# Optimization experiments

Measured on AMD Instinct MI355X. Metric: run time of the kernel, lower is better.

## Reference

```python
import jax, jax.numpy as jnp
import numpy as np

D_MODEL = 512
NUM_HEADS = 8
HEAD_DIM = D_MODEL // NUM_HEADS
NEG_INF = -1e9


def setup_inputs() -> dict:
    key = jax.random.key(0)
    ks = jax.random.split(key, 12)
    B, S = 4, 2048
    std = 1.0 / np.sqrt(D_MODEL)
    inp = {
        "query": jax.random.normal(ks[0], (B, S, D_MODEL), jnp.float32),
        "key": jax.random.normal(ks[1], (B, S, D_MODEL), jnp.float32),
        "value": jax.random.normal(ks[2], (B, S, D_MODEL), jnp.float32),
        "mask": jax.random.randint(ks[3], (B, 1, S, S), 0, 2, jnp.int32),
        "Wq": jax.random.normal(ks[4], (D_MODEL, D_MODEL), jnp.float32) * std,
        "bq": jnp.zeros((D_MODEL,), jnp.float32),
        "Wk": jax.random.normal(ks[5], (D_MODEL, D_MODEL), jnp.float32) * std,
        "bk": jnp.zeros((D_MODEL,), jnp.float32),
        "Wv": jax.random.normal(ks[6], (D_MODEL, D_MODEL), jnp.float32) * std,
        "bv": jnp.zeros((D_MODEL,), jnp.float32),
        "Wo": jax.random.normal(ks[7], (D_MODEL, D_MODEL), jnp.float32) * std,
        "bo": jnp.zeros((D_MODEL,), jnp.float32),
    }
    return inp


def _split_heads(x):
    B, S, _ = x.shape
    return x.reshape(B, S, NUM_HEADS, HEAD_DIM).transpose(0, 2, 1, 3)  # [B,H,S,Dh]


def reference(query, key, value, mask, Wq, bq, Wk, bk, Wv, bv, Wo, bo):
    B, S, _ = query.shape
    q = _split_heads(query @ Wq + bq)
    k = _split_heads(key @ Wk + bk)
    v = _split_heads(value @ Wv + bv)
    # scores: [B,H,S,S]
    scores = jnp.einsum("bhqd,bhkd->bhqk", q, k) / jnp.sqrt(jnp.float32(HEAD_DIM))
    scores = jnp.where(mask == 0, jnp.float32(NEG_INF), scores)
    attn = jax.nn.softmax(scores, axis=-1)  # dropout p=0 -> identity
    out = jnp.einsum("bhqk,bhkd->bhqd", attn, v)
    out = out.transpose(0, 2, 1, 3).reshape(B, S, D_MODEL)
    return out @ Wo + bo
```

## Files before the change

kernel.cpp:

```cpp
#include <hip/hip_runtime.h>

typedef unsigned short u16;
typedef __attribute__((ext_vector_type(4))) float f32x4;
typedef __attribute__((ext_vector_type(8))) short s16x8;
typedef __attribute__((ext_vector_type(4))) unsigned short u16x4;

__device__ __forceinline__ u16 f2bf(float f) {
    union { float f; unsigned u; } v; v.f = f;
    unsigned r = v.u + 0x7fffu + ((v.u >> 16) & 1u);
    return (u16)(r >> 16);
}
__device__ __forceinline__ float bf2f(u16 h) {
    union { unsigned u; float f; } v; v.u = ((unsigned)h) << 16;
    return v.f;
}
__device__ __forceinline__ void gload16(const void* g, void* lds_uniform) {
    __builtin_amdgcn_global_load_lds(
        (const __attribute__((address_space(1))) void*)g,
        (__attribute__((address_space(3))) void*)lds_uniform, 16, 0, 0);
}
__device__ __forceinline__ f32x4 mfma16(s16x8 a, s16x8 b, f32x4 c) {
    return __builtin_amdgcn_mfma_f32_16x16x32_bf16(a, b, c, 0, 0, 0);
}

__global__ void cvtbf3(const float4* __restrict__ q, const float4* __restrict__ k,
                       const float4* __restrict__ v, u16x4* __restrict__ out) {
    int i = blockIdx.x * 256 + threadIdx.x;
    int sel = i >> 20;
    int j = i & 0xFFFFF;
    const float4* in = (sel == 0) ? q : (sel == 1) ? k : v;
    float4 f = in[j];
    u16x4 o;
    o[0] = f2bf(f.x); o[1] = f2bf(f.y); o[2] = f2bf(f.z); o[3] = f2bf(f.w);
    out[i] = o;
}

__global__ void wtrans(const float* __restrict__ W0, const float* __restrict__ W1,
                       const float* __restrict__ W2, const float* __restrict__ W3,
                       u16* __restrict__ T0, u16* __restrict__ T1,
                       u16* __restrict__ T2, u16* __restrict__ T3) {
    const float* W; u16* T;
    switch (blockIdx.z) {
        case 0: W = W0; T = T0; break;
        case 1: W = W1; T = T1; break;
        case 2: W = W2; T = T2; break;
        default: W = W3; T = T3; break;
    }
    __shared__ float tile[32][33];
    const int tx = threadIdx.x & 31, ty = threadIdx.x >> 5;
    const int k0 = blockIdx.y * 32, n0 = blockIdx.x * 32;
#pragma unroll
    for (int r = 0; r < 32; r += 8) tile[ty + r][tx] = W[(k0 + ty + r) * 512 + n0 + tx];
    __syncthreads();
#pragma unroll
    for (int r = 0; r < 32; r += 8) T[(n0 + ty + r) * 512 + k0 + tx] = f2bf(tile[tx][ty + r]);
}

__global__ void packmask(const int* __restrict__ mask, unsigned* __restrict__ bits) {
    int i = blockIdx.x * 256 + threadIdx.x;
    int v = mask[i];
    unsigned long long bal = __ballot(v != 0);
    if ((threadIdx.x & 63) == 0) {
        uint2 w; w.x = (unsigned)bal; w.y = (unsigned)(bal >> 32);
        *(uint2*)&bits[i >> 5] = w;
    }
}

template <int BIAS_ROW, int OUT_F32>
__global__ __launch_bounds__(256, 2) void gemm_bt(
    const u16* __restrict__ A, const u16* __restrict__ Bt0, const u16* __restrict__ Bt1,
    const float* __restrict__ bias0, const float* __restrict__ bias1,
    void* __restrict__ Cout, int M, int N, int K, int ysplit) {
    const u16* Bt = (blockIdx.y < (unsigned)ysplit) ? Bt0 : Bt1;
    const float* bias = (blockIdx.y < (unsigned)ysplit) ? bias0 : bias1;
    __shared__ u16 As[128 * 32];
    __shared__ u16 Bs[128 * 32];
    const int t = threadIdx.x, l = t & 63, w = t >> 6;
    const int lr = l & 15, lg = l >> 4;
    const int m0 = blockIdx.y * 128, n0 = blockIdx.x * 128;
    const int wr = w >> 1, wc = w & 1;
    f32x4 acc[4][4] = {};

    const int c0 = t, c1 = 256 + t;
    const int ar0 = c0 >> 2, ac0 = (c0 & 3) * 8;
    const int ar1 = c1 >> 2, ac1 = (c1 & 3) * 8;

    for (int kk = 0; kk < K; kk += 32) {
        __syncthreads();
        gload16(A + (m0 + ar0) * K + kk + ac0, As + (w * 64) * 8);
        gload16(A + (m0 + ar1) * K + kk + ac1, As + (256 + w * 64) * 8);
        gload16(Bt + (n0 + ar0) * K + kk + ac0, Bs + (w * 64) * 8);
        gload16(Bt + (n0 + ar1) * K + kk + ac1, Bs + (256 + w * 64) * 8);
        __syncthreads();
        s16x8 af[4], bf[4];
#pragma unroll
        for (int m = 0; m < 4; ++m)
            af[m] = *(const s16x8*)&As[(wr * 64 + m * 16 + lr) * 32 + lg * 8];
#pragma unroll
        for (int n = 0; n < 4; ++n)
            bf[n] = *(const s16x8*)&Bs[(wc * 64 + n * 16 + lr) * 32 + lg * 8];
#pragma unroll
        for (int m = 0; m < 4; ++m)
#pragma unroll
            for (int n = 0; n < 4; ++n) acc[m][n] = mfma16(af[m], bf[n], acc[m][n]);
    }

#pragma unroll
    for (int n = 0; n < 4; ++n) {
        const int cg = n0 + wc * 64 + n * 16 + lr;
        const float bcol = BIAS_ROW ? 0.f : bias[cg];
#pragma unroll
        for (int m = 0; m < 4; ++m) {
            const int rbase = m0 + wr * 64 + m * 16 + lg * 4;
#pragma unroll
            for (int j = 0; j < 4; ++j) {
                const int rg = rbase + j;
                float v = acc[m][n][j] + (BIAS_ROW ? bias[rg] : bcol);
                if (OUT_F32) ((float*)Cout)[rg * N + cg] = v;
                else         ((u16*)Cout)[rg * N + cg] = f2bf(v);
            }
        }
    }
}

__global__ __launch_bounds__(256, 4) void attn_fwd(
    const u16* __restrict__ Qp, const u16* __restrict__ Kp,
    const u16* __restrict__ Vt, const unsigned* __restrict__ mbits,
    u16* __restrict__ AO) {
    constexpr int S = 2048;
    const int qt = blockIdx.x, bh = blockIdx.y;
    const int b = bh >> 3, h = bh & 7;
    const int t = threadIdx.x, l = t & 63, w = t >> 6;
    const int lr = l & 15, lg = l >> 4;

    __shared__ u16 Ks[64 * 64];
    __shared__ u16 Vs[64 * 64];
    __shared__ u16 Ps[4][16 * 64];

    const int q0 = qt * 64 + w * 16;
    const int bS = b * S;

    s16x8 qf[2];
#pragma unroll
    for (int ks = 0; ks < 2; ++ks) {
        s16x8 v = *(const s16x8*)&Qp[(bS + q0 + lr) * 512 + h * 64 + ks * 32 + lg * 8];
#pragma unroll
        for (int j = 0; j < 8; ++j) v[j] = (short)f2bf(bf2f((u16)v[j]) * 0.125f);
        qf[ks] = v;
    }

    f32x4 po[4] = {};
    float lrun[4] = {0.f, 0.f, 0.f, 0.f};

    const int kc0 = t, kc1 = 256 + t;
    const int krow0 = kc0 >> 3, kcol0 = ((kc0 & 7) ^ (krow0 & 7)) * 8;
    const int krow1 = kc1 >> 3, kcol1 = ((kc1 & 7) ^ (krow1 & 7)) * 8;

    for (int kt0 = 0; kt0 < S; kt0 += 64) {
        __syncthreads();
        gload16(&Kp[(bS + kt0 + krow0) * 512 + h * 64 + kcol0], &Ks[w * 512]);
        gload16(&Kp[(bS + kt0 + krow1) * 512 + h * 64 + kcol1], &Ks[2048 + w * 512]);
        gload16(&Vt[(h * 64 + krow0) * (4 * S) + bS + kt0 + kcol0], &Vs[w * 512]);
        gload16(&Vt[(h * 64 + krow1) * (4 * S) + bS + kt0 + kcol1], &Vs[2048 + w * 512]);

        uint2 mw[4];
#pragma unroll
        for (int jj = 0; jj < 4; ++jj)
            mw[jj] = *(const uint2*)&mbits[(bS + q0 + lg * 4 + jj) * 64 + (kt0 >> 5)];
        __syncthreads();

        f32x4 sc[4];
#pragma unroll
        for (int nk = 0; nk < 4; ++nk) sc[nk] = f32x4{0.f, 0.f, 0.f, 0.f};
#pragma unroll
        for (int nk = 0; nk < 4; ++nk) {
            const int ktc = nk * 16 + lr;
            const int sw = (ktc & 7) << 4;
            s16x8 k0 = *(const s16x8*)((const char*)Ks + ((ktc * 128 + lg * 16) ^ sw));
            s16x8 k1 = *(const s16x8*)((const char*)Ks + ((ktc * 128 + 64 + lg * 16) ^ sw));
            sc[nk] = mfma16(qf[0], k0, sc[nk]);
            sc[nk] = mfma16(qf[1], k1, sc[nk]);
        }

#pragma unroll
        for (int nk = 0; nk < 4; ++nk) {
            const unsigned bp = ((nk & 1) << 4) + lr;
#pragma unroll
            for (int jj = 0; jj < 4; ++jj) {
                const unsigned word = (nk >> 1) ? mw[jj].y : mw[jj].x;
                const float s = ((word >> bp) & 1u) ? sc[nk][jj] : -1e9f;
                sc[nk][jj] = __expf(s);
            }
        }
#pragma unroll
        for (int jj = 0; jj < 4; ++jj)
            lrun[jj] += (sc[0][jj] + sc[1][jj]) + (sc[2][jj] + sc[3][jj]);

#pragma unroll
        for (int nk = 0; nk < 4; ++nk) {
            const int ktc = nk * 16 + lr;
#pragma unroll
            for (int jj = 0; jj < 4; ++jj) {
                const int qloc = lg * 4 + jj;
                const int byte = (qloc * 128 + ktc * 2) ^ ((qloc & 7) << 4);
                *(u16*)((char*)&Ps[w][0] + byte) = f2bf(sc[nk][jj]);
            }
        }

        s16x8 pa[2];
#pragma unroll
        for (int k2 = 0; k2 < 2; ++k2) {
            const int byte = (lr * 128 + k2 * 64 + lg * 16) ^ ((lr & 7) << 4);
            pa[k2] = *(const s16x8*)((const char*)&Ps[w][0] + byte);
        }
#pragma unroll
        for (int dn = 0; dn < 4; ++dn) {
            const int d = dn * 16 + lr;
            const int sw = (d & 7) << 4;
            s16x8 v0 = *(const s16x8*)((const char*)Vs + ((d * 128 + lg * 16) ^ sw));
            s16x8 v1 = *(const s16x8*)((const char*)Vs + ((d * 128 + 64 + lg * 16) ^ sw));
            po[dn] = mfma16(pa[0], v0, po[dn]);
            po[dn] = mfma16(pa[1], v1, po[dn]);
        }
    }

#pragma unroll
    for (int jj = 0; jj < 4; ++jj) {
        float s = lrun[jj];
        s += __shfl_xor(s, 1);
        s += __shfl_xor(s, 2);
        s += __shfl_xor(s, 4);
        s += __shfl_xor(s, 8);
        const float inv = 1.f / s;
        const int q = q0 + lg * 4 + jj;
#pragma unroll
        for (int dn = 0; dn < 4; ++dn)
            AO[(bS + q) * 512 + h * 64 + dn * 16 + lr] = f2bf(po[dn][jj] * inv);
    }
}

extern "C" void kernel_launch(void* const* d_in, const int* in_sizes, int n_in,
                              void* d_out, int out_size, void* d_ws, size_t ws_size,
                              hipStream_t stream) {
    (void)in_sizes; (void)n_in; (void)out_size; (void)ws_size;
    const float* query = (const float*)d_in[0];
    const float* key   = (const float*)d_in[1];
    const float* value = (const float*)d_in[2];
    const int*   mask  = (const int*)d_in[3];
    const float* Wq = (const float*)d_in[4];
    const float* bq = (const float*)d_in[5];
    const float* Wk = (const float*)d_in[6];
    const float* bk = (const float*)d_in[7];
    const float* Wv = (const float*)d_in[8];
    const float* bv = (const float*)d_in[9];
    const float* Wo = (const float*)d_in[10];
    const float* bo = (const float*)d_in[11];

    char* ws = (char*)d_ws;
    const size_t MB = 1ull << 20;
    u16* qb  = (u16*)(ws);
    u16* vb  = (u16*)(ws + 16 * MB);
    u16* WqT = (u16*)(ws + 24 * MB);
    u16* WkT = (u16*)(ws + 24 * MB + 512 * 1024);
    u16* WvT = (u16*)(ws + 25 * MB);
    u16* WoT = (u16*)(ws + 25 * MB + 512 * 1024);
    unsigned* mb = (unsigned*)(ws + 26 * MB);
    u16* Qp = (u16*)(ws + 28 * MB);
    u16* Vt = (u16*)(ws + 44 * MB);
    u16* AO = (u16*)(ws + 52 * MB);

    cvtbf3<<<12288, 256, 0, stream>>>((const float4*)query, (const float4*)key,
                                      (const float4*)value, (u16x4*)qb);
    wtrans<<<dim3(16, 16, 4), 256, 0, stream>>>(Wq, Wk, Wv, Wo, WqT, WkT, WvT, WoT);
    packmask<<<65536, 256, 0, stream>>>(mask, mb);

    gemm_bt<0, 0><<<dim3(4, 128), 256, 0, stream>>>(qb, WqT, WkT, bq, bk, Qp,
                                                    16384, 512, 512, 64);
    gemm_bt<1, 0><<<dim3(64, 4), 256, 0, stream>>>(WvT, vb, vb, bv, bv, Vt,
                                                   512, 8192, 512, 999);

    attn_fwd<<<dim3(32, 32), 256, 0, stream>>>(Qp, Qp + 8192 * 512, Vt, mb, AO);

    gemm_bt<0, 1><<<dim3(4, 64), 256, 0, stream>>>(AO, WoT, WoT, bo, bo,
                                                   (float*)d_out, 8192, 512, 512, 999);
}
```

Baseline: 159.5 us.

## Fuse preprocessing kernels, shrink GEMM tiles, and use exp2 with folded log2e scale

```diff
diff --git a/kernel.cpp b/kernel.cpp
--- a/kernel.cpp
+++ b/kernel.cpp
@@ -14,6 +14,13 @@
     union { unsigned u; float f; } v; v.u = ((unsigned)h) << 16;
     return v.f;
 }
+__device__ __forceinline__ float fexp2(float x) {
+#if __has_builtin(__builtin_amdgcn_exp2f)
+    return __builtin_amdgcn_exp2f(x);
+#else
+    return exp2f(x);
+#endif
+}
 __device__ __forceinline__ void gload16(const void* g, void* lds_uniform) {
     __builtin_amdgcn_global_load_lds(
         (const __attribute__((address_space(1))) void*)g,
@@ -23,101 +30,101 @@
     return __builtin_amdgcn_mfma_f32_16x16x32_bf16(a, b, c, 0, 0, 0);
 }
 
-__global__ void cvtbf3(const float4* __restrict__ q, const float4* __restrict__ k,
-                       const float4* __restrict__ v, u16x4* __restrict__ out) {
-    int i = blockIdx.x * 256 + threadIdx.x;
-    int sel = i >> 20;
-    int j = i & 0xFFFFF;
-    const float4* in = (sel == 0) ? q : (sel == 1) ? k : v;
-    float4 f = in[j];
-    u16x4 o;
-    o[0] = f2bf(f.x); o[1] = f2bf(f.y); o[2] = f2bf(f.z); o[3] = f2bf(f.w);
-    out[i] = o;
-}
-
-__global__ void wtrans(const float* __restrict__ W0, const float* __restrict__ W1,
-                       const float* __restrict__ W2, const float* __restrict__ W3,
-                       u16* __restrict__ T0, u16* __restrict__ T1,
-                       u16* __restrict__ T2, u16* __restrict__ T3) {
-    const float* W; u16* T;
-    switch (blockIdx.z) {
-        case 0: W = W0; T = T0; break;
-        case 1: W = W1; T = T1; break;
-        case 2: W = W2; T = T2; break;
-        default: W = W3; T = T3; break;
-    }
+__global__ void prep(const float4* __restrict__ q, const float4* __restrict__ k,
+                     const float4* __restrict__ v, u16x4* __restrict__ qkv,
+                     const float* __restrict__ Wq, const float* __restrict__ Wk,
+                     const float* __restrict__ Wv, const float* __restrict__ Wo,
+                     u16* __restrict__ WqT, u16* __restrict__ WkT,
+                     u16* __restrict__ WvT, u16* __restrict__ WoT,
+                     const int* __restrict__ mask, unsigned* __restrict__ bits) {
     __shared__ float tile[32][33];
-    const int tx = threadIdx.x & 31, ty = threadIdx.x >> 5;
-    const int k0 = blockIdx.y * 32, n0 = blockIdx.x * 32;
-#pragma unroll
-    for (int r = 0; r < 32; r += 8) tile[ty + r][tx] = W[(k0 + ty + r) * 512 + n0 + tx];
-    __syncthreads();
-#pragma unroll
-    for (int r = 0; r < 32; r += 8) T[(n0 + ty + r) * 512 + k0 + tx] = f2bf(tile[tx][ty + r]);
-}
-
-__global__ void packmask(const int* __restrict__ mask, unsigned* __restrict__ bits) {
-    int i = blockIdx.x * 256 + threadIdx.x;
-    int v = mask[i];
-    unsigned long long bal = __ballot(v != 0);
-    if ((threadIdx.x & 63) == 0) {
-        uint2 w; w.x = (unsigned)bal; w.y = (unsigned)(bal >> 32);
-        *(uint2*)&bits[i >> 5] = w;
-    }
-}
-
-template <int BIAS_ROW, int OUT_F32>
-__global__ __launch_bounds__(256, 2) void gemm_bt(
+    const int bid = blockIdx.x, tid = threadIdx.x;
+    if (bid < 12288) {
+        int i = bid * 256 + tid;
+        int sel = i >> 20, j = i & 0xFFFFF;
+        const float4* in = (sel == 0) ? q : (sel == 1) ? k : v;
+        float4 f = in[j];
+        u16x4 o;
+        o[0] = f2bf(f.x); o[1] = f2bf(f.y); o[2] = f2bf(f.z); o[3] = f2bf(f.w);
+        qkv[i] = o;
+    } else if (bid < 13312) {
+        int idx = bid - 12288;
+        int bz = idx >> 8, rem = idx & 255, by = rem >> 4, bx = rem & 15;
+        const float* W; u16* T;
+        switch (bz) {
+            case 0: W = Wq; T = WqT; break;
+            case 1: W = Wk; T = WkT; break;
+            case 2: W = Wv; T = WvT; break;
+            default: W = Wo; T = WoT; break;
+        }
+        const int tx = tid & 31, ty = tid >> 5;
+        const int k0 = by * 32, n0 = bx * 32;
+#pragma unroll
+        for (int r = 0; r < 32; r += 8) tile[ty + r][tx] = W[(k0 + ty + r) * 512 + n0 + tx];
+        __syncthreads();
+#pragma unroll
+        for (int r = 0; r < 32; r += 8) T[(n0 + ty + r) * 512 + k0 + tx] = f2bf(tile[tx][ty + r]);
+    } else {
+        int i = (bid - 13312) * 256 + tid;
+        int m = mask[i];
+        unsigned long long bal = __ballot(m != 0);
+        if ((tid & 63) == 0) {
+            uint2 w2; w2.x = (unsigned)bal; w2.y = (unsigned)(bal >> 32);
+            *(uint2*)&bits[i >> 5] = w2;
+        }
+    }
+}
+
+template <int BM, int BIAS_ROW, int OUT_F32>
+__global__ __launch_bounds__(256, 4) void gemm_bt(
     const u16* __restrict__ A, const u16* __restrict__ Bt0, const u16* __restrict__ Bt1,
     const float* __restrict__ bias0, const float* __restrict__ bias1,
     void* __restrict__ Cout, int M, int N, int K, int ysplit) {
+    constexpr int MR = BM / 32;
     const u16* Bt = (blockIdx.y < (unsigned)ysplit) ? Bt0 : Bt1;
     const float* bias = (blockIdx.y < (unsigned)ysplit) ? bias0 : bias1;
-    __shared__ u16 As[128 * 32];
-    __shared__ u16 Bs[128 * 32];
+    __shared__ u16 As[BM * 32];
+    __shared__ u16 Bs[64 * 32];
     const int t = threadIdx.x, l = t & 63, w = t >> 6;
     const int lr = l & 15, lg = l >> 4;
-    const int m0 = blockIdx.y * 128, n0 = blockIdx.x * 128;
+    const int m0 = blockIdx.y * BM, n0 = blockIdx.x * 64;
     const int wr = w >> 1, wc = w & 1;
-    f32x4 acc[4][4] = {};
-
-    const int c0 = t, c1 = 256 + t;
-    const int ar0 = c0 >> 2, ac0 = (c0 & 3) * 8;
-    const int ar1 = c1 >> 2, ac1 = (c1 & 3) * 8;
+    f32x4 acc[MR][2] = {};
+    const int ar = t >> 2, ac = (t & 3) * 8;
 
     for (int kk = 0; kk < K; kk += 32) {
         __syncthreads();
-        gload16(A + (m0 + ar0) * K + kk + ac0, As + (w * 64) * 8);
-        gload16(A + (m0 + ar1) * K + kk + ac1, As + (256 + w * 64) * 8);
-        gload16(Bt + (n0 + ar0) * K + kk + ac0, Bs + (w * 64) * 8);
-        gload16(Bt + (n0 + ar1) * K + kk + ac1, Bs + (256 + w * 64) * 8);
-        __syncthreads();
-        s16x8 af[4], bf[4];
-#pragma unroll
-        for (int m = 0; m < 4; ++m)
-            af[m] = *(const s16x8*)&As[(wr * 64 + m * 16 + lr) * 32 + lg * 8];
-#pragma unroll
-        for (int n = 0; n < 4; ++n)
-            bf[n] = *(const s16x8*)&Bs[(wc * 64 + n * 16 + lr) * 32 + lg * 8];
-#pragma unroll
-        for (int m = 0; m < 4; ++m)
-#pragma unroll
-            for (int n = 0; n < 4; ++n) acc[m][n] = mfma16(af[m], bf[n], acc[m][n]);
-    }
-
-#pragma unroll
-    for (int n = 0; n < 4; ++n) {
-        const int cg = n0 + wc * 64 + n * 16 + lr;
+        gload16(A + (m0 + ar) * K + kk + ac, As + w * 512);
+        if (BM == 128)
+            gload16(A + (m0 + 64 + ar) * K + kk + ac, As + 2048 + w * 512);
+        gload16(Bt + (n0 + ar) * K + kk + ac, Bs + w * 512);
+        __syncthreads();
+        s16x8 af[MR], bfr[2];
+#pragma unroll
+        for (int m = 0; m < MR; ++m)
+            af[m] = *(const s16x8*)&As[(wr * (BM / 2) + m * 16 + lr) * 32 + lg * 8];
+#pragma unroll
+        for (int n = 0; n < 2; ++n)
+            bfr[n] = *(const s16x8*)&Bs[(wc * 32 + n * 16 + lr) * 32 + lg * 8];
+#pragma unroll
+        for (int m = 0; m < MR; ++m)
+#pragma unroll
+            for (int n = 0; n < 2; ++n) acc[m][n] = mfma16(af[m], bfr[n], acc[m][n]);
+    }
+
+#pragma unroll
+    for (int n = 0; n < 2; ++n) {
+        const int cg = n0 + wc * 32 + n * 16 + lr;
         const float bcol = BIAS_ROW ? 0.f : bias[cg];
 #pragma unroll
-        for (int m = 0; m < 4; ++m) {
-            const int rbase = m0 + wr * 64 + m * 16 + lg * 4;
+        for (int m = 0; m < MR; ++m) {
+            const int rbase = m0 + wr * (BM / 2) + m * 16 + lg * 4;
 #pragma unroll
             for (int j = 0; j < 4; ++j) {
                 const int rg = rbase + j;
-                float v = acc[m][n][j] + (BIAS_ROW ? bias[rg] : bcol);
-                if (OUT_F32) ((float*)Cout)[rg * N + cg] = v;
-                else         ((u16*)Cout)[rg * N + cg] = f2bf(v);
+                float val = acc[m][n][j] + (BIAS_ROW ? bias[rg] : bcol);
+                if (OUT_F32) ((float*)Cout)[(size_t)rg * N + cg] = val;
+                else         ((u16*)Cout)[(size_t)rg * N + cg] = f2bf(val);
             }
         }
     }
@@ -145,7 +152,7 @@
     for (int ks = 0; ks < 2; ++ks) {
         s16x8 v = *(const s16x8*)&Qp[(bS + q0 + lr) * 512 + h * 64 + ks * 32 + lg * 8];
 #pragma unroll
-        for (int j = 0; j < 8; ++j) v[j] = (short)f2bf(bf2f((u16)v[j]) * 0.125f);
+        for (int j = 0; j < 8; ++j) v[j] = (short)f2bf(bf2f((u16)v[j]) * 0.1803368851f);
         qf[ks] = v;
     }
 
@@ -189,7 +196,7 @@
             for (int jj = 0; jj < 4; ++jj) {
                 const unsigned word = (nk >> 1) ? mw[jj].y : mw[jj].x;
                 const float s = ((word >> bp) & 1u) ? sc[nk][jj] : -1e9f;
-                sc[nk][jj] = __expf(s);
+                sc[nk][jj] = fexp2(s);
             }
         }
 #pragma unroll
@@ -213,6 +220,7 @@
             const int byte = (lr * 128 + k2 * 64 + lg * 16) ^ ((lr & 7) << 4);
             pa[k2] = *(const s16x8*)((const char*)&Ps[w][0] + byte);
         }
+
 #pragma unroll
         for (int dn = 0; dn < 4; ++dn) {
             const int d = dn * 16 + lr;
@@ -269,18 +277,17 @@
     u16* Vt = (u16*)(ws + 44 * MB);
     u16* AO = (u16*)(ws + 52 * MB);
 
-    cvtbf3<<<12288, 256, 0, stream>>>((const float4*)query, (const float4*)key,
-                                      (const float4*)value, (u16x4*)qb);
-    wtrans<<<dim3(16, 16, 4), 256, 0, stream>>>(Wq, Wk, Wv, Wo, WqT, WkT, WvT, WoT);
-    packmask<<<65536, 256, 0, stream>>>(mask, mb);
-
-    gemm_bt<0, 0><<<dim3(4, 128), 256, 0, stream>>>(qb, WqT, WkT, bq, bk, Qp,
-                                                    16384, 512, 512, 64);
-    gemm_bt<1, 0><<<dim3(64, 4), 256, 0, stream>>>(WvT, vb, vb, bv, bv, Vt,
-                                                   512, 8192, 512, 999);
+    prep<<<78848, 256, 0, stream>>>((const float4*)query, (const float4*)key,
+                                    (const float4*)value, (u16x4*)qb,
+                                    Wq, Wk, Wv, Wo, WqT, WkT, WvT, WoT, mask, mb);
+
+    gemm_bt<128, 0, 0><<<dim3(8, 128), 256, 0, stream>>>(qb, WqT, WkT, bq, bk, Qp,
+                                                         16384, 512, 512, 64);
+    gemm_bt<64, 1, 0><<<dim3(128, 8), 256, 0, stream>>>(WvT, vb, vb, bv, bv, Vt,
+                                                        512, 8192, 512, 999);
 
     attn_fwd<<<dim3(32, 32), 256, 0, stream>>>(Qp, Qp + 8192 * 512, Vt, mb, AO);
 
-    gemm_bt<0, 1><<<dim3(4, 64), 256, 0, stream>>>(AO, WoT, WoT, bo, bo,
-                                                   (float*)d_out, 8192, 512, 512, 999);
-}
+    gemm_bt<64, 0, 1><<<dim3(8, 128), 256, 0, stream>>>(AO, WoT, WoT, bo, bo,
+                                                        (float*)d_out, 8192, 512, 512, 999);
+}
```

Result: faster. 156.3 us (-2.0%).
